# Optimization experiments

Measured on AMD Instinct MI355X. Metric: run time of the kernel, lower is better.

## Reference

```python
import math
import jax, jax.numpy as jnp
import numpy as np

L, W, H, T, B = 12, 1024, 16, 1024, 2
CH = W // H  # per-head channels
SCALE = 1.0 / math.sqrt(math.sqrt(CH))
STD = 0.25 * math.sqrt(1.0 / W)  # init_scale * sqrt(1/width)


def setup_inputs() -> dict:
    key = jax.random.key(0)
    ks = jax.random.split(key, 8)
    x = jax.random.normal(ks[0], (B, T, W), dtype=jnp.float32)
    qkv_w = jax.random.normal(ks[1], (L, W, 3 * W), dtype=jnp.float32) * STD
    qkv_b = jnp.zeros((L, 3 * W), jnp.float32)
    proj_w = jax.random.normal(ks[2], (L, W, W), dtype=jnp.float32) * STD
    proj_b = jnp.zeros((L, W), jnp.float32)
    ln1_g = jnp.ones((L, W), jnp.float32)
    ln1_b = jnp.zeros((L, W), jnp.float32)
    ln2_g = jnp.ones((L, W), jnp.float32)
    ln2_b = jnp.zeros((L, W), jnp.float32)
    fc_w = jax.random.normal(ks[3], (L, W, 4 * W), dtype=jnp.float32) * STD
    fc_b = jnp.zeros((L, 4 * W), jnp.float32)
    fc2_w = jax.random.normal(ks[4], (L, 4 * W, W), dtype=jnp.float32) * STD
    fc2_b = jnp.zeros((L, W), jnp.float32)
    return dict(x=x, qkv_w=qkv_w, qkv_b=qkv_b, proj_w=proj_w, proj_b=proj_b,
                ln1_g=ln1_g, ln1_b=ln1_b, ln2_g=ln2_g, ln2_b=ln2_b,
                fc_w=fc_w, fc_b=fc_b, fc2_w=fc2_w, fc2_b=fc2_b)


def _ln(x, g, b, eps=1e-5):
    mu = jnp.mean(x, axis=-1, keepdims=True)
    var = jnp.mean(jnp.square(x - mu), axis=-1, keepdims=True)
    return (x - mu) * jax.lax.rsqrt(var + eps) * g + b


def _attn(h, w_qkv, b_qkv, w_p, b_p):
    bs, t, w = h.shape
    qkv = (h @ w_qkv + b_qkv).reshape(bs, t, H, 3 * CH)
    q, k, v = jnp.split(qkv, 3, axis=-1)  # each [bs, t, H, CH]
    # double-sqrt scaling as in QKVMultiheadAttention
    wts = jnp.einsum('bthc,bshc->bhts', q * SCALE, k * SCALE)
    wts = jax.nn.softmax(wts.astype(jnp.float32), axis=-1).astype(h.dtype)
    o = jnp.einsum('bhts,bshc->bthc', wts, v).reshape(bs, t, w)
    return o @ w_p + b_p


def reference(x, qkv_w, qkv_b, proj_w, proj_b, ln1_g, ln1_b, ln2_g, ln2_b,
              fc_w, fc_b, fc2_w, fc2_b):
    def step(h, p):
        wq, bq, wp, bp, g1, b1, g2, b2, wf, bf, w2, b2m = p
        h = h + _attn(_ln(h, g1, b1), wq, bq, wp, bp)
        z = _ln(h, g2, b2)
        h = h + (jax.nn.gelu(z @ wf + bf, approximate=False) @ w2 + b2m)
        return h, None
    params = (qkv_w, qkv_b, proj_w, proj_b, ln1_g, ln1_b, ln2_g, ln2_b,
              fc_w, fc_b, fc2_w, fc2_b)
    out, _ = jax.lax.scan(step, x, params)
    return out
```

## Files before the change

### kernel.cpp

```cpp
#include <hip/hip_runtime.h>
#include <hip/hip_bf16.h>
#include <math.h>

typedef __bf16 bf16;
typedef __bf16 bf16x8 __attribute__((ext_vector_type(8)));
typedef __bf16 bf16x4 __attribute__((ext_vector_type(4)));
typedef float  f32x4  __attribute__((ext_vector_type(4)));

#define DEV __device__ __forceinline__

DEV void lds_load16(const void* g, void* l) {
  __builtin_amdgcn_global_load_lds(
      (__attribute__((address_space(1))) unsigned int*)g,
      (__attribute__((address_space(3))) unsigned int*)l, 16, 0, 0);
}

DEV f32x4 mfma16(bf16x8 a, bf16x8 b, f32x4 c) {
  return __builtin_amdgcn_mfma_f32_16x16x32_bf16(a, b, c, 0, 0, 0);
}

DEV int xcd_swz(int flat, int nwg) {
  int q = nwg >> 3, r = nwg & 7;
  int xcd = flat & 7, idx = flat >> 3;
  return (xcd < r ? xcd * (q + 1) : r * (q + 1) + (xcd - r) * q) + idx;
}

__global__ __launch_bounds__(256) void transpose_cvt(
    const float* __restrict__ in0, bf16* __restrict__ out0, int R, int C) {
  __shared__ float t[64][65];
  size_t zo = (size_t)blockIdx.z * R * C;
  const float* in = in0 + zo;
  bf16* out = out0 + zo;
  int c0 = blockIdx.x * 64, r0 = blockIdx.y * 64;
  int tr = threadIdx.x >> 4, tc4 = (threadIdx.x & 15) * 4;
#pragma unroll
  for (int i = 0; i < 4; i++) {
    float4 v = *(const float4*)(in + (size_t)(r0 + tr + i * 16) * C + c0 + tc4);
    t[tr + i * 16][tc4 + 0] = v.x;
    t[tr + i * 16][tc4 + 1] = v.y;
    t[tr + i * 16][tc4 + 2] = v.z;
    t[tr + i * 16][tc4 + 3] = v.w;
  }
  __syncthreads();
  int oc = threadIdx.x >> 2, j = threadIdx.x & 3;
  bf16x8 o0, o1;
#pragma unroll
  for (int i = 0; i < 8; i++) o0[i] = (bf16)t[j * 16 + i][oc];
#pragma unroll
  for (int i = 0; i < 8; i++) o1[i] = (bf16)t[j * 16 + 8 + i][oc];
  bf16* op = out + (size_t)(c0 + oc) * R + r0 + j * 16;
  *(bf16x8*)op = o0;
  *(bf16x8*)(op + 8) = o1;
}

__global__ __launch_bounds__(256) void ln_fwd(
    const float* __restrict__ x, const float* __restrict__ gw,
    const float* __restrict__ bw, bf16* __restrict__ y,
    float* __restrict__ hout) {
  int row = blockIdx.x, tid = threadIdx.x;
  const float4 v = ((const float4*)(x + (size_t)row * 1024))[tid];
  if (hout) ((float4*)(hout + (size_t)row * 1024))[tid] = v;
  float s  = v.x + v.y + v.z + v.w;
  float s2 = v.x * v.x + v.y * v.y + v.z * v.z + v.w * v.w;
#pragma unroll
  for (int o = 1; o < 64; o <<= 1) {
    s  += __shfl_xor(s, o);
    s2 += __shfl_xor(s2, o);
  }
  __shared__ float ps[4], ps2[4];
  int wv = tid >> 6;
  if ((tid & 63) == 0) { ps[wv] = s; ps2[wv] = s2; }
  __syncthreads();
  s  = ps[0] + ps[1] + ps[2] + ps[3];
  s2 = ps2[0] + ps2[1] + ps2[2] + ps2[3];
  float mu  = s * (1.f / 1024.f);
  float var = s2 * (1.f / 1024.f) - mu * mu;
  float rs  = rsqrtf(var + 1e-5f);
  float4 gv = ((const float4*)gw)[tid];
  float4 bv = ((const float4*)bw)[tid];
  bf16x4 o4;
  o4[0] = (bf16)((v.x - mu) * rs * gv.x + bv.x);
  o4[1] = (bf16)((v.y - mu) * rs * gv.y + bv.y);
  o4[2] = (bf16)((v.z - mu) * rs * gv.z + bv.z);
  o4[3] = (bf16)((v.w - mu) * rs * gv.w + bv.w);
  *(bf16x4*)(y + (size_t)row * 1024 + tid * 4) = o4;
}

__global__ __launch_bounds__(256) void reduce_ln(
    const bf16* __restrict__ parts, int nparts, const float* __restrict__ bias,
    float* __restrict__ h, const float* __restrict__ gw,
    const float* __restrict__ bw, bf16* __restrict__ y) {
  const int row = blockIdx.x, tid = threadIdx.x;
  const size_t MN = (size_t)gridDim.x * 1024;
  const size_t eoff = (size_t)row * 1024 + tid * 4;
  float sx = 0.f, sy = 0.f, sz = 0.f, sw = 0.f;
  for (int p = 0; p < nparts; p++) {
    bf16x4 v = *(const bf16x4*)(parts + (size_t)p * MN + eoff);
    sx += (float)v[0]; sy += (float)v[1]; sz += (float)v[2]; sw += (float)v[3];
  }
  const size_t rb = (size_t)row * 256;
  const float4 bb = ((const float4*)bias)[tid];
  float4 r = ((float4*)h)[rb + tid];
  r.x += sx + bb.x; r.y += sy + bb.y; r.z += sz + bb.z; r.w += sw + bb.w;
  ((float4*)h)[rb + tid] = r;
  if (gw == nullptr) return;
  float sm  = r.x + r.y + r.z + r.w;
  float sm2 = r.x * r.x + r.y * r.y + r.z * r.z + r.w * r.w;
#pragma unroll
  for (int o = 1; o < 64; o <<= 1) {
    sm  += __shfl_xor(sm, o);
    sm2 += __shfl_xor(sm2, o);
  }
  __shared__ float ps[4], ps2[4];
  int wv = tid >> 6;
  if ((tid & 63) == 0) { ps[wv] = sm; ps2[wv] = sm2; }
  __syncthreads();
  sm  = ps[0] + ps[1] + ps[2] + ps[3];
  sm2 = ps2[0] + ps2[1] + ps2[2] + ps2[3];
  float mu  = sm * (1.f / 1024.f);
  float var = sm2 * (1.f / 1024.f) - mu * mu;
  float rs  = rsqrtf(var + 1e-5f);
  float4 gv = ((const float4*)gw)[tid];
  float4 bv = ((const float4*)bw)[tid];
  bf16x4 o4;
  o4[0] = (bf16)((r.x - mu) * rs * gv.x + bv.x);
  o4[1] = (bf16)((r.y - mu) * rs * gv.y + bv.y);
  o4[2] = (bf16)((r.z - mu) * rs * gv.z + bv.z);
  o4[3] = (bf16)((r.w - mu) * rs * gv.w + bv.w);
  *(bf16x4*)(y + (size_t)row * 1024 + tid * 4) = o4;
}

template <int EPI>
__global__ __launch_bounds__(512, 2) void gemm8p(
    const bf16* __restrict__ A, const bf16* __restrict__ Bt,
    const float* __restrict__ bias, bf16* __restrict__ outb,
    int M, int N, int K, int kcount) {
  __shared__ __align__(16) char lds[3 * 49152];
  const int tid = threadIdx.x, wv = tid >> 6, lane = tid & 63;
  const int g = lane >> 4, lr = lane & 15;
  const int wr = wv >> 2, wc = wv & 3;
  const int nwg = gridDim.x * gridDim.y;
  const int wgid = xcd_swz(blockIdx.y * gridDim.x + blockIdx.x, nwg);
  const int bn = wgid % gridDim.x, bm = wgid / gridDim.x;
  const int kbegin = blockIdx.z * kcount;
  const bf16* Ab = A + (size_t)bm * 128 * K + kbegin;
  const bf16* Bb = Bt + (size_t)bn * 256 * K + kbegin;
  const int nt = kcount >> 6;

  f32x4 acc[4][4] = {};

  auto stageA = [&](int t) {
    char* dst = lds + (t % 3) * 49152;
    int k0 = t * 64;
#pragma unroll
    for (int c = 0; c < 2; c++) {
      int off = c * 8192 + tid * 16;
      int row = off >> 7, cb = off & 127;
      int cbs = cb ^ ((row & 7) << 4);
      lds_load16((const char*)(Ab + (size_t)row * K + k0) + cbs, dst + off);
    }
  };
  auto stageB = [&](int t, int half) {
    char* dst = lds + (t % 3) * 49152 + 16384 + half * 16384;
    int k0 = t * 64;
#pragma unroll
    for (int c = 0; c < 2; c++) {
      int off = c * 8192 + tid * 16;
      int row = (off >> 7) + half * 128, cb = off & 127;
      int cbs = cb ^ ((row & 7) << 4);
      lds_load16((const char*)(Bb + (size_t)row * K + k0) + cbs, dst + off);
    }
  };
  auto ldA = [&](int t, int m, int kk) -> bf16x8 {
    const char* base = lds + (t % 3) * 49152;
    int row = wr * 64 + m * 16 + lr;
    int col = (kk * 64 + g * 16) ^ ((row & 7) << 4);
    return *(const bf16x8*)(base + row * 128 + col);
  };
  auto ldB = [&](int t, int n, int kk) -> bf16x8 {
    const char* base = lds + (t % 3) * 49152 + 16384;
    int row = wc * 64 + n * 16 + lr;
    int col = (kk * 64 + g * 16) ^ ((row & 7) << 4);
    return *(const bf16x8*)(base + row * 128 + col);
  };

  stageA(0); stageB(0, 0); stageB(0, 1);
  if (nt > 1) {
    stageA(1); stageB(1, 0); stageB(1, 1);
    asm volatile("s_waitcnt vmcnt(6)" ::: "memory");
  } else {
    asm volatile("s_waitcnt vmcnt(0)" ::: "memory");
  }
  __builtin_amdgcn_s_barrier();

  bf16x8 a[4][2], b[4][2];
  for (int t = 0; t < nt; ++t) {
#pragma unroll
    for (int m = 0; m < 4; m++)
#pragma unroll
      for (int kk = 0; kk < 2; kk++) a[m][kk] = ldA(t, m, kk);
#pragma unroll
    for (int n = 0; n < 2; n++)
#pragma unroll
      for (int kk = 0; kk < 2; kk++) b[n][kk] = ldB(t, n, kk);
    if (t + 2 < nt) { stageA(t + 2); stageB(t + 2, 0); }
    __builtin_amdgcn_s_barrier();
    asm volatile("s_waitcnt lgkmcnt(0)" ::: "memory");
    __builtin_amdgcn_sched_barrier(0);
    __builtin_amdgcn_s_setprio(1);
#pragma unroll
    for (int m = 0; m < 4; m++)
#pragma unroll
      for (int n = 0; n < 2; n++)
#pragma unroll
        for (int kk = 0; kk < 2; kk++)
          acc[m][n] = mfma16(a[m][kk], b[n][kk], acc[m][n]);
    __builtin_amdgcn_s_setprio(0);
    __builtin_amdgcn_s_barrier();
#pragma unroll
    for (int n = 2; n < 4; n++)
#pragma unroll
      for (int kk = 0; kk < 2; kk++) b[n][kk] = ldB(t, n, kk);
    if (t + 2 < nt) {
      stageB(t + 2, 1);
      asm volatile("s_waitcnt vmcnt(6)" ::: "memory");
    } else if (t + 1 < nt) {
      asm volatile("s_waitcnt vmcnt(0)" ::: "memory");
    }
    __builtin_amdgcn_s_barrier();
    asm volatile("s_waitcnt lgkmcnt(0)" ::: "memory");
    __builtin_amdgcn_sched_barrier(0);
    __builtin_amdgcn_s_setprio(1);
#pragma unroll
    for (int m = 0; m < 4; m++)
#pragma unroll
      for (int n = 2; n < 4; n++)
#pragma unroll
        for (int kk = 0; kk < 2; kk++)
          acc[m][n] = mfma16(a[m][kk], b[n][kk], acc[m][n]);
    __builtin_amdgcn_s_setprio(0);
    __builtin_amdgcn_s_barrier();
  }

  bf16* ob = (EPI == 3) ? outb + (size_t)blockIdx.z * M * N : outb;
#pragma unroll
  for (int m = 0; m < 4; m++) {
#pragma unroll
    for (int n = 0; n < 4; n++) {
      int col = bn * 256 + wc * 64 + n * 16 + lr;
      float bv = (EPI == 3) ? 0.f : bias[col];
#pragma unroll
      for (int r = 0; r < 4; r++) {
        int row = bm * 128 + wr * 64 + m * 16 + g * 4 + r;
        size_t idx = (size_t)row * N + col;
        float v = acc[m][n][r] + bv;
        if (EPI == 2) {
          ob[idx] = (bf16)(0.5f * v * (1.f + erff(v * 0.70710678118f)));
        } else {
          ob[idx] = (bf16)v;
        }
      }
    }
  }
}

__global__ __launch_bounds__(256) void attn_fwd(
    const bf16* __restrict__ qkv, bf16* __restrict__ outp) {
  __shared__ __align__(16) bf16 Kls[2][128 * 64];
  __shared__ __align__(16) bf16 Vt[2][64 * 128];
  __shared__ __align__(16) bf16 Pls[4 * 16 * 128];
  const int tid = threadIdx.x, wv = tid >> 6, lane = tid & 63;
  const int g = lane >> 4, lr = lane & 15;
  const int wgid = xcd_swz(blockIdx.y * gridDim.x + blockIdx.x,
                           gridDim.x * gridDim.y);
  const int bh = wgid / gridDim.x, bb = bh >> 4, hh = bh & 15;
  const int q0 = (wgid % gridDim.x) * 64;
  const bf16* base = qkv + (size_t)bb * 1024 * 3072;
  const int qc = hh * 192, kc = qc + 64, vc = qc + 128;

  auto kstage = [&](int t, int buf) {
#pragma unroll
    for (int c = 0; c < 4; c++) {
      int off = wv * 4096 + c * 1024 + lane * 16;
      int s = off >> 7, cb = off & 127;
      int cbs = cb ^ ((s & 7) << 4);
      lds_load16(
          (const char*)(base + (size_t)(t * 128 + s) * 3072 + kc) + cbs,
          (char*)Kls[buf] + off);
    }
  };

  bf16x8 aq[2];
  {
    int row = q0 + wv * 16 + lr;
#pragma unroll
    for (int kk = 0; kk < 2; kk++) {
      bf16x8 v = *(const bf16x8*)(base + (size_t)row * 3072 + qc + kk * 32 + g * 8);
#pragma unroll
      for (int j = 0; j < 8; j++) v[j] = (bf16)((float)v[j] * 0.1803368801f);
      aq[kk] = v;
    }
  }

  f32x4 o[4] = {};
  float rm[4], rl[4];
#pragma unroll
  for (int r = 0; r < 4; r++) { rm[r] = -1e30f; rl[r] = 0.f; }

  kstage(0, 0);
#pragma unroll
  for (int it = 0; it < 2; it++) {
    int idx = it * 256 + tid;
    int s = (idx >> 3) * 2, c0i = (idx & 7) * 8;
    bf16x8 v0 = *(const bf16x8*)(base + (size_t)s * 3072 + vc + c0i);
    bf16x8 v1 = *(const bf16x8*)(base + (size_t)(s + 1) * 3072 + vc + c0i);
#pragma unroll
    for (int j = 0; j < 8; j++) {
      int c = c0i + j;
      unsigned int pk = (unsigned int)__builtin_bit_cast(unsigned short, v0[j]) |
                        ((unsigned int)__builtin_bit_cast(unsigned short, v1[j]) << 16);
      *(unsigned int*)((char*)Vt[0] + c * 256 + ((s * 2) ^ ((c & 7) << 4))) = pk;
    }
  }

  for (int ti = 0; ti < 8; ++ti) {
    const int cur = ti & 1, nxt = cur ^ 1;
    __syncthreads();
    f32x4 sa[8] = {};
#pragma unroll
    for (int kk = 0; kk < 2; kk++) {
#pragma unroll
      for (int n = 0; n < 8; n++) {
        int srow = n * 16 + lr;
        int cbyte = (kk * 32 + g * 8) * 2;
        bf16x8 kb = *(const bf16x8*)((char*)Kls[cur] + srow * 128 +
                                     (cbyte ^ ((srow & 7) << 4)));
        sa[n] = mfma16(aq[kk], kb, sa[n]);
      }
    }
    bf16x8 vreg[2][2];
    if (ti + 1 < 8) {
      kstage(ti + 1, nxt);
#pragma unroll
      for (int it = 0; it < 2; it++) {
        int idx = it * 256 + tid;
        int s = (idx >> 3) * 2, c0i = (idx & 7) * 8;
        vreg[it][0] = *(const bf16x8*)(
            base + (size_t)((ti + 1) * 128 + s) * 3072 + vc + c0i);
        vreg[it][1] = *(const bf16x8*)(
            base + (size_t)((ti + 1) * 128 + s + 1) * 3072 + vc + c0i);
      }
    }
    float al[4];
#pragma unroll
    for (int r = 0; r < 4; r++) {
      float tm = -1e30f;
#pragma unroll
      for (int n = 0; n < 8; n++) tm = fmaxf(tm, sa[n][r]);
      tm = fmaxf(tm, __shfl_xor(tm, 1));
      tm = fmaxf(tm, __shfl_xor(tm, 2));
      tm = fmaxf(tm, __shfl_xor(tm, 4));
      tm = fmaxf(tm, __shfl_xor(tm, 8));
      if (tm - rm[r] <= 11.0f) {
        al[r] = 1.0f;
      } else {
        al[r] = exp2f(rm[r] - tm);
        rm[r] = tm;
      }
    }
    float psum[4] = {0.f, 0.f, 0.f, 0.f};
#pragma unroll
    for (int n = 0; n < 8; n++) {
#pragma unroll
      for (int r = 0; r < 4; r++) {
        float p = exp2f(sa[n][r] - rm[r]);
        psum[r] += p;
        int rw = g * 4 + r;
        int sb = (n * 16 + lr) * 2;
        *(bf16*)((char*)Pls + wv * 4096 + rw * 256 + (sb ^ ((rw & 7) << 4))) =
            (bf16)p;
      }
    }
#pragma unroll
    for (int r = 0; r < 4; r++) {
      psum[r] += __shfl_xor(psum[r], 1);
      psum[r] += __shfl_xor(psum[r], 2);
      psum[r] += __shfl_xor(psum[r], 4);
      psum[r] += __shfl_xor(psum[r], 8);
      rl[r] = rl[r] * al[r] + psum[r];
      if (al[r] != 1.0f) {
#pragma unroll
        for (int n = 0; n < 4; n++) o[n][r] *= al[r];
      }
    }
    asm volatile("s_waitcnt lgkmcnt(0)" ::: "memory");
    __builtin_amdgcn_sched_barrier(0);
#pragma unroll
    for (int sc = 0; sc < 4; sc++) {
      int sb = (sc * 32 + g * 8) * 2;
      bf16x8 pa = *(const bf16x8*)((char*)Pls + wv * 4096 + lr * 256 +
                                   (sb ^ ((lr & 7) << 4)));
#pragma unroll
      for (int n = 0; n < 4; n++) {
        int c = n * 16 + lr;
        bf16x8 vb = *(const bf16x8*)((char*)Vt[cur] + c * 256 +
                                     (sb ^ ((c & 7) << 4)));
        o[n] = mfma16(pa, vb, o[n]);
      }
    }
    if (ti + 1 < 8) {
#pragma unroll
      for (int it = 0; it < 2; it++) {
        int idx = it * 256 + tid;
        int s = (idx >> 3) * 2, c0i = (idx & 7) * 8;
#pragma unroll
        for (int j = 0; j < 8; j++) {
          int c = c0i + j;
          unsigned int pk =
              (unsigned int)__builtin_bit_cast(unsigned short, vreg[it][0][j]) |
              ((unsigned int)__builtin_bit_cast(unsigned short, vreg[it][1][j])
               << 16);
          *(unsigned int*)((char*)Vt[nxt] + c * 256 + ((s * 2) ^ ((c & 7) << 4))) =
              pk;
        }
      }
    }
  }
#pragma unroll
  for (int n = 0; n < 4; n++)
#pragma unroll
    for (int r = 0; r < 4; r++) {
      int row = q0 + wv * 16 + g * 4 + r;
      int col = hh * 64 + n * 16 + lr;
      outp[(size_t)(bb * 1024 + row) * 1024 + col] = (bf16)(o[n][r] / rl[r]);
    }
}

extern "C" void kernel_launch(void* const* d_in, const int* in_sizes, int n_in,
                              void* d_out, int out_size, void* d_ws,
                              size_t ws_size, hipStream_t stream) {
  const float* x      = (const float*)d_in[0];
  const float* qkv_w  = (const float*)d_in[1];
  const float* qkv_b  = (const float*)d_in[2];
  const float* proj_w = (const float*)d_in[3];
  const float* proj_b = (const float*)d_in[4];
  const float* ln1_g  = (const float*)d_in[5];
  const float* ln1_b  = (const float*)d_in[6];
  const float* ln2_g  = (const float*)d_in[7];
  const float* ln2_b  = (const float*)d_in[8];
  const float* fc_w   = (const float*)d_in[9];
  const float* fc_b   = (const float*)d_in[10];
  const float* fc2_w  = (const float*)d_in[11];
  const float* fc2_b  = (const float*)d_in[12];
  float* h = (float*)d_out;

  char* ws = (char*)d_ws;
  size_t off = 0;
  auto alloc = [&](size_t bytes) -> char* {
    char* p = ws + off;
    off = (off + bytes + 255) & ~(size_t)255;
    return p;
  };
  bf16* wq_t    = (bf16*)alloc((size_t)12 * 3072 * 1024 * 2);
  bf16* wp_t    = (bf16*)alloc((size_t)12 * 1024 * 1024 * 2);
  bf16* wf_t    = (bf16*)alloc((size_t)12 * 4096 * 1024 * 2);
  bf16* w2_t    = (bf16*)alloc((size_t)12 * 1024 * 4096 * 2);
  bf16* lnbuf   = (bf16*)alloc((size_t)2048 * 1024 * 2);
  bf16* qkvbuf  = (bf16*)alloc((size_t)2048 * 3072 * 2);
  bf16* attnbuf = (bf16*)alloc((size_t)2048 * 1024 * 2);
  bf16* fcbuf   = (bf16*)alloc((size_t)2048 * 4096 * 2);
  bf16* partbuf = (bf16*)alloc((size_t)4 * 2048 * 1024 * 2);

  transpose_cvt<<<dim3(48, 16, 12), 256, 0, stream>>>(qkv_w, wq_t, 1024, 3072);
  transpose_cvt<<<dim3(16, 16, 12), 256, 0, stream>>>(proj_w, wp_t, 1024, 1024);
  transpose_cvt<<<dim3(64, 16, 12), 256, 0, stream>>>(fc_w, wf_t, 1024, 4096);
  transpose_cvt<<<dim3(16, 64, 12), 256, 0, stream>>>(fc2_w, w2_t, 4096, 1024);

  ln_fwd<<<2048, 256, 0, stream>>>(x, ln1_g, ln1_b, lnbuf, h);

  for (int l = 0; l < 12; l++) {
    const bf16* wq = wq_t + (size_t)l * 3072 * 1024;
    const bf16* wp = wp_t + (size_t)l * 1024 * 1024;
    const bf16* wf = wf_t + (size_t)l * 4096 * 1024;
    const bf16* w2 = w2_t + (size_t)l * 1024 * 4096;

    gemm8p<0><<<dim3(12, 16, 1), 512, 0, stream>>>(
        lnbuf, wq, qkv_b + (size_t)l * 3072, qkvbuf, 2048, 3072, 1024, 1024);
    attn_fwd<<<dim3(16, 32), 256, 0, stream>>>(qkvbuf, attnbuf);
    gemm8p<3><<<dim3(4, 16, 4), 512, 0, stream>>>(
        attnbuf, wp, nullptr, partbuf, 2048, 1024, 1024, 256);
    reduce_ln<<<2048, 256, 0, stream>>>(partbuf, 4, proj_b + (size_t)l * 1024,
                                        h, ln2_g + (size_t)l * 1024,
                                        ln2_b + (size_t)l * 1024, lnbuf);
    gemm8p<2><<<dim3(16, 16, 1), 512, 0, stream>>>(
        lnbuf, wf, fc_b + (size_t)l * 4096, fcbuf, 2048, 4096, 1024, 1024);
    gemm8p<3><<<dim3(4, 16, 4), 512, 0, stream>>>(
        fcbuf, w2, nullptr, partbuf, 2048, 1024, 4096, 1024);
    if (l < 11) {
      reduce_ln<<<2048, 256, 0, stream>>>(
          partbuf, 4, fc2_b + (size_t)l * 1024, h,
          ln1_g + (size_t)(l + 1) * 1024, ln1_b + (size_t)(l + 1) * 1024,
          lnbuf);
    } else {
      reduce_ln<<<2048, 256, 0, stream>>>(partbuf, 4,
                                          fc2_b + (size_t)l * 1024, h, nullptr,
                                          nullptr, nullptr);
    }
  }
}
```

Measured before the change: 1.765 ms.

## Use 256x256-tile split-K GEMM with 8-way K split for FC2 projection

Adds a new gemm256 kernel with 256x256 output tiles, 128KB double-buffered LDS, and two k-substeps per 64-wide stage. The FC2 GEMM now runs on it with an 8-way K split over a 4x8x8 grid, and partial buffers and the reduce_ln fan-in double to 8. The larger tile raises arithmetic intensity and cuts operand reloads from global memory. The cost is more partial-sum traffic and reduction work, heavy register use for 32 accumulators per wave, and occupancy limited to one block per CU by the LDS size.

```diff
diff --git a/kernel.cpp b/kernel.cpp
--- a/kernel.cpp
+++ b/kernel.cpp
@@ -264,6 +264,109 @@
   }
 }
 
+__global__ __launch_bounds__(512) void gemm256(
+    const bf16* __restrict__ A, const bf16* __restrict__ Bt,
+    bf16* __restrict__ outb, int M, int N, int K, int kcount) {
+  __shared__ __align__(16) char lds[2 * 65536];
+  const int tid = threadIdx.x, wv = tid >> 6, lane = tid & 63;
+  const int g = lane >> 4, lr = lane & 15;
+  const int wr = wv >> 2, wc = wv & 3;
+  const int nwg = gridDim.x * gridDim.y;
+  const int wgid = xcd_swz(blockIdx.y * gridDim.x + blockIdx.x, nwg);
+  const int bn = wgid % gridDim.x, bm = wgid / gridDim.x;
+  const int kbegin = blockIdx.z * kcount;
+  const bf16* Ab = A + (size_t)bm * 256 * K + kbegin;
+  const bf16* Bb = Bt + (size_t)bn * 256 * K + kbegin;
+  const int nt = kcount >> 6;
+  f32x4 acc[8][4] = {};
+
+  auto stage = [&](int t) {
+    char* dst = lds + (t & 1) * 65536;
+#pragma unroll
+    for (int c = 0; c < 4; c++) {
+      int off = c * 8192 + tid * 16;
+      int row = off >> 7, cb = off & 127;
+      int cbs = cb ^ ((row & 7) << 4);
+      lds_load16((const char*)(Ab + (size_t)row * K + t * 64) + cbs, dst + off);
+    }
+#pragma unroll
+    for (int c = 0; c < 4; c++) {
+      int off = c * 8192 + tid * 16;
+      int row = off >> 7, cb = off & 127;
+      int cbs = cb ^ ((row & 7) << 4);
+      lds_load16((const char*)(Bb + (size_t)row * K + t * 64) + cbs,
+                 dst + 32768 + off);
+    }
+  };
+  auto ldA = [&](int t, int m, int kk) -> bf16x8 {
+    const char* base = lds + (t & 1) * 65536;
+    int row = wr * 128 + m * 16 + lr;
+    int col = (kk * 64 + g * 16) ^ ((row & 7) << 4);
+    return *(const bf16x8*)(base + row * 128 + col);
+  };
+  auto ldB = [&](int t, int n, int kk) -> bf16x8 {
+    const char* base = lds + (t & 1) * 65536 + 32768;
+    int row = wc * 64 + n * 16 + lr;
+    int col = (kk * 64 + g * 16) ^ ((row & 7) << 4);
+    return *(const bf16x8*)(base + row * 128 + col);
+  };
+
+  stage(0);
+  if (nt > 1) stage(1);
+
+  for (int t = 0; t < nt; ++t) {
+    if (t + 1 < nt)
+      asm volatile("s_waitcnt vmcnt(8)" ::: "memory");
+    else
+      asm volatile("s_waitcnt vmcnt(0)" ::: "memory");
+    __builtin_amdgcn_s_barrier();
+    bf16x8 a[8], b[4];
+#pragma unroll
+    for (int m = 0; m < 8; m++) a[m] = ldA(t, m, 0);
+#pragma unroll
+    for (int n = 0; n < 4; n++) b[n] = ldB(t, n, 0);
+    asm volatile("s_waitcnt lgkmcnt(0)" ::: "memory");
+    __builtin_amdgcn_sched_barrier(0);
+    __builtin_amdgcn_s_setprio(1);
+#pragma unroll
+    for (int m = 0; m < 8; m++)
+#pragma unroll
+      for (int n = 0; n < 4; n++)
+        acc[m][n] = mfma16(a[m], b[n], acc[m][n]);
+    __builtin_amdgcn_s_setprio(0);
+#pragma unroll
+    for (int m = 0; m < 8; m++) a[m] = ldA(t, m, 1);
+#pragma unroll
+    for (int n = 0; n < 4; n++) b[n] = ldB(t, n, 1);
+    asm volatile("s_waitcnt lgkmcnt(0)" ::: "memory");
+    __builtin_amdgcn_sched_barrier(0);
+    __builtin_amdgcn_s_barrier();
+    if (t + 2 < nt) stage(t + 2);
+    __builtin_amdgcn_sched_barrier(0);
+    __builtin_amdgcn_s_setprio(1);
+#pragma unroll
+    for (int m = 0; m < 8; m++)
+#pragma unroll
+      for (int n = 0; n < 4; n++)
+        acc[m][n] = mfma16(a[m], b[n], acc[m][n]);
+    __builtin_amdgcn_s_setprio(0);
+  }
+
+  bf16* ob = outb + (size_t)blockIdx.z * M * N;
+#pragma unroll
+  for (int m = 0; m < 8; m++) {
+#pragma unroll
+    for (int n = 0; n < 4; n++) {
+      int col = bn * 256 + wc * 64 + n * 16 + lr;
+#pragma unroll
+      for (int r = 0; r < 4; r++) {
+        int row = bm * 256 + wr * 128 + m * 16 + g * 4 + r;
+        ob[(size_t)row * N + col] = (bf16)acc[m][n][r];
+      }
+    }
+  }
+}
+
 __global__ __launch_bounds__(256) void attn_fwd(
     const bf16* __restrict__ qkv, bf16* __restrict__ outp) {
   __shared__ __align__(16) bf16 Kls[2][128 * 64];
@@ -469,7 +572,7 @@
   bf16* qkvbuf  = (bf16*)alloc((size_t)2048 * 3072 * 2);
   bf16* attnbuf = (bf16*)alloc((size_t)2048 * 1024 * 2);
   bf16* fcbuf   = (bf16*)alloc((size_t)2048 * 4096 * 2);
-  bf16* partbuf = (bf16*)alloc((size_t)4 * 2048 * 1024 * 2);
+  bf16* partbuf = (bf16*)alloc((size_t)8 * 2048 * 1024 * 2);
 
   transpose_cvt<<<dim3(48, 16, 12), 256, 0, stream>>>(qkv_w, wq_t, 1024, 3072);
   transpose_cvt<<<dim3(16, 16, 12), 256, 0, stream>>>(proj_w, wp_t, 1024, 1024);
@@ -494,15 +597,15 @@
                                         ln2_b + (size_t)l * 1024, lnbuf);
     gemm8p<2><<<dim3(16, 16, 1), 512, 0, stream>>>(
         lnbuf, wf, fc_b + (size_t)l * 4096, fcbuf, 2048, 4096, 1024, 1024);
-    gemm8p<3><<<dim3(4, 16, 4), 512, 0, stream>>>(
-        fcbuf, w2, nullptr, partbuf, 2048, 1024, 4096, 1024);
+    gemm256<<<dim3(4, 8, 8), 512, 0, stream>>>(
+        fcbuf, w2, partbuf, 2048, 1024, 4096, 512);
     if (l < 11) {
       reduce_ln<<<2048, 256, 0, stream>>>(
-          partbuf, 4, fc2_b + (size_t)l * 1024, h,
+          partbuf, 8, fc2_b + (size_t)l * 1024, h,
           ln1_g + (size_t)(l + 1) * 1024, ln1_b + (size_t)(l + 1) * 1024,
           lnbuf);
     } else {
-      reduce_ln<<<2048, 256, 0, stream>>>(partbuf, 4,
+      reduce_ln<<<2048, 256, 0, stream>>>(partbuf, 8,
                                           fc2_b + (size_t)l * 1024, h, nullptr,
                                           nullptr, nullptr);
     }
```

Result: slower. 1.817 ms (+3.0%).

## Add 128x128-tile 4-wave GEMM with triple-buffered LDS for proj/fc/fc2

Applied to the files above, without the earlier changes.

Adds a new GEMM kernel, gemm4w, that uses 128x128 tiles, 256 threads, a 3-slot LDS ring buffer with global_load_lds prefetch two stages ahead, and an XOR swizzle. Launch bounds allow 3 workgroups per CU. The proj, fc and fc2 GEMMs now use it, while the QKV GEMM keeps the original kernel with its epilogue reduced to bias-only. The intent is more workgroups and better occupancy on the 256-CU part, overlapping loads with MFMA, in exchange for less data reuse per tile.

```diff
diff --git a/kernel.cpp b/kernel.cpp
--- a/kernel.cpp
+++ b/kernel.cpp
@@ -242,12 +242,103 @@
     __builtin_amdgcn_s_barrier();
   }
 
-  bf16* ob = (EPI == 3) ? outb + (size_t)blockIdx.z * M * N : outb;
 #pragma unroll
   for (int m = 0; m < 4; m++) {
 #pragma unroll
     for (int n = 0; n < 4; n++) {
       int col = bn * 256 + wc * 64 + n * 16 + lr;
+      float bv = bias[col];
+#pragma unroll
+      for (int r = 0; r < 4; r++) {
+        int row = bm * 128 + wr * 64 + m * 16 + g * 4 + r;
+        outb[(size_t)row * N + col] = (bf16)(acc[m][n][r] + bv);
+      }
+    }
+  }
+}
+
+template <int EPI>
+__global__ __launch_bounds__(256, 3) void gemm4w(
+    const bf16* __restrict__ A, const bf16* __restrict__ Bt,
+    const float* __restrict__ bias, bf16* __restrict__ outb,
+    int M, int N, int K, int kcount) {
+  constexpr int SLOT = (128 + 128) * 32 * 2;
+  __shared__ __align__(16) char lds[3 * SLOT];
+  const int tid = threadIdx.x, wv = tid >> 6, lane = tid & 63;
+  const int g = lane >> 4, lr = lane & 15;
+  const int wr = wv >> 1, wc = wv & 1;
+  const int nwg = gridDim.x * gridDim.y;
+  const int wgid = xcd_swz(blockIdx.y * gridDim.x + blockIdx.x, nwg);
+  const int bn = wgid % gridDim.x, bm = wgid / gridDim.x;
+  const int kbegin = blockIdx.z * kcount;
+  const bf16* Ab = A + (size_t)bm * 128 * K + kbegin;
+  const bf16* Bb = Bt + (size_t)bn * 128 * K + kbegin;
+  const int nt = kcount >> 5;
+  f32x4 acc[4][4] = {};
+
+  auto stage = [&](int t) {
+    char* dst = lds + (t % 3) * SLOT;
+#pragma unroll
+    for (int c = 0; c < 2; c++) {
+      int off = c * 4096 + tid * 16;
+      int row = off >> 6, cb = off & 63;
+      int cbs = cb ^ (((row >> 1) & 3) << 4);
+      lds_load16((const char*)(Ab + (size_t)row * K + t * 32) + cbs, dst + off);
+    }
+#pragma unroll
+    for (int c = 0; c < 2; c++) {
+      int off = c * 4096 + tid * 16;
+      int row = off >> 6, cb = off & 63;
+      int cbs = cb ^ (((row >> 1) & 3) << 4);
+      lds_load16((const char*)(Bb + (size_t)row * K + t * 32) + cbs,
+                 dst + 8192 + off);
+    }
+  };
+  auto ldA = [&](int t, int m) -> bf16x8 {
+    const char* base = lds + (t % 3) * SLOT;
+    int row = wr * 64 + m * 16 + lr;
+    int col = (g * 16) ^ (((row >> 1) & 3) << 4);
+    return *(const bf16x8*)(base + row * 64 + col);
+  };
+  auto ldB = [&](int t, int n) -> bf16x8 {
+    const char* base = lds + (t % 3) * SLOT + 8192;
+    int row = wc * 64 + n * 16 + lr;
+    int col = (g * 16) ^ (((row >> 1) & 3) << 4);
+    return *(const bf16x8*)(base + row * 64 + col);
+  };
+
+  stage(0);
+  stage(1);
+
+  for (int t = 0; t < nt; ++t) {
+    if (t + 1 < nt)
+      asm volatile("s_waitcnt vmcnt(4)" ::: "memory");
+    else
+      asm volatile("s_waitcnt vmcnt(0)" ::: "memory");
+    __builtin_amdgcn_s_barrier();
+    bf16x8 a[4], b[4];
+#pragma unroll
+    for (int m = 0; m < 4; m++) a[m] = ldA(t, m);
+#pragma unroll
+    for (int n = 0; n < 4; n++) b[n] = ldB(t, n);
+    if (t + 2 < nt) stage(t + 2);
+    asm volatile("s_waitcnt lgkmcnt(0)" ::: "memory");
+    __builtin_amdgcn_sched_barrier(0);
+    __builtin_amdgcn_s_setprio(1);
+#pragma unroll
+    for (int m = 0; m < 4; m++)
+#pragma unroll
+      for (int n = 0; n < 4; n++)
+        acc[m][n] = mfma16(a[m], b[n], acc[m][n]);
+    __builtin_amdgcn_s_setprio(0);
+  }
+
+  bf16* ob = (EPI == 3) ? outb + (size_t)blockIdx.z * M * N : outb;
+#pragma unroll
+  for (int m = 0; m < 4; m++) {
+#pragma unroll
+    for (int n = 0; n < 4; n++) {
+      int col = bn * 128 + wc * 64 + n * 16 + lr;
       float bv = (EPI == 3) ? 0.f : bias[col];
 #pragma unroll
       for (int r = 0; r < 4; r++) {
@@ -487,14 +578,14 @@
     gemm8p<0><<<dim3(12, 16, 1), 512, 0, stream>>>(
         lnbuf, wq, qkv_b + (size_t)l * 3072, qkvbuf, 2048, 3072, 1024, 1024);
     attn_fwd<<<dim3(16, 32), 256, 0, stream>>>(qkvbuf, attnbuf);
-    gemm8p<3><<<dim3(4, 16, 4), 512, 0, stream>>>(
+    gemm4w<3><<<dim3(8, 16, 4), 256, 0, stream>>>(
         attnbuf, wp, nullptr, partbuf, 2048, 1024, 1024, 256);
     reduce_ln<<<2048, 256, 0, stream>>>(partbuf, 4, proj_b + (size_t)l * 1024,
                                         h, ln2_g + (size_t)l * 1024,
                                         ln2_b + (size_t)l * 1024, lnbuf);
-    gemm8p<2><<<dim3(16, 16, 1), 512, 0, stream>>>(
+    gemm4w<2><<<dim3(32, 16, 1), 256, 0, stream>>>(
         lnbuf, wf, fc_b + (size_t)l * 4096, fcbuf, 2048, 4096, 1024, 1024);
-    gemm8p<3><<<dim3(4, 16, 4), 512, 0, stream>>>(
+    gemm4w<3><<<dim3(8, 16, 4), 256, 0, stream>>>(
         fcbuf, w2, nullptr, partbuf, 2048, 1024, 4096, 1024);
     if (l < 11) {
       reduce_ln<<<2048, 256, 0, stream>>>(
```

Result: slower. 1.841 ms (+4.3%).
